# Performance work log

Measured on AMD Instinct MI355X. Metric: run time of the kernel, lower is better.

## Reference

```python
import jax, jax.numpy as jnp
import numpy as np

SR = 22050
FRAME_LENGTH = 64
ATTENUATE_GAIN = 0.02


def upsample_linear(x, scale):
    """torch nn.Upsample(mode='linear', align_corners=False) along last axis."""
    T = x.shape[-1]
    S = T * scale
    # source coordinate for each output sample (half-pixel convention), clamped
    coords = jnp.clip((jnp.arange(S, dtype=jnp.float32) + 0.5) / scale - 0.5, 0.0, T - 1)
    i0 = jnp.floor(coords).astype(jnp.int32)
    i1 = jnp.minimum(i0 + 1, T - 1)
    w = (coords - i0).astype(x.dtype)
    return x[..., i0] * (1.0 - w) + x[..., i1] * w


def setup_inputs() -> dict:
    key = jax.random.key(0)
    k1, k2, k3 = jax.random.split(key, 3)
    B, T, P, STR = 16, 1000, 64, 6
    # fundamental frequencies in [50, 450] Hz so high partials hit the Nyquist mask
    six_f0 = jax.random.uniform(k1, (B, T, STR), dtype=jnp.float32) * 400.0 + 50.0
    c = jax.random.uniform(k2, (STR, B, P, T), dtype=jnp.float32)
    a = jax.random.uniform(k3, (STR, B, T), dtype=jnp.float32)
    return {"six_f0": six_f0, "c": c, "a": a, "string_idx": 1}


def reference(six_f0, c, a, string_idx):
    sidx = string_idx - 1
    fundamentals = six_f0[..., sidx]        # (B, T)
    c_bank = c[sidx]                        # (B, P, T)
    loudness = a[sidx]                      # (B, T)
    P = c_bank.shape[1]

    partial_mult = jnp.arange(1, P + 1, dtype=jnp.float32)[:, None]   # (P, 1)
    f0_bank = fundamentals[:, None, :] * partial_mult                  # (B, P, T)
    mask = (f0_bank < SR / 2).astype(c_bank.dtype)
    c_masked = c_bank * mask

    f0_up = upsample_linear(f0_bank, FRAME_LENGTH)                     # (B, P, S)
    phase = jnp.cumsum(f0_up / SR, axis=2)
    a_up = upsample_linear(c_masked, FRAME_LENGTH)                     # (B, P, S)
    sinusoid_bank = jnp.sin(2.0 * np.pi * phase) * a_up * ATTENUATE_GAIN

    loudness_up = upsample_linear(loudness, FRAME_LENGTH)              # (B, S)
    return jnp.sum(sinusoid_bank, axis=1) * loudness_up                # (B, S)
```

## Files before the change

### kernel.cpp

```cpp
#include <hip/hip_runtime.h>
#include <math.h>

constexpr int B = 16, T = 1000, P = 64, STR = 6, SCALE = 64;
constexpr int S = T * SCALE;
constexpr int SEG_PITCH = 1024;
constexpr int SEGS_PER_BLK = 16;
constexpr int NF = 17;
constexpr int NBLK = 63;
#define NYQ 11025.0f
#define INV_SR (1.0f / 22050.0f)

__device__ __forceinline__ float fracf_(float x) {
#if __has_builtin(__builtin_amdgcn_fractf)
  return __builtin_amdgcn_fractf(x);
#else
  return x - floorf(x);
#endif
}
__device__ __forceinline__ float sin2pi(float r) {
#if __has_builtin(__builtin_amdgcn_sinf)
  return __builtin_amdgcn_sinf(r);
#else
  return __sinf(r * 6.28318530717958647692f);
#endif
}
__device__ __forceinline__ float cos2pi(float r) {
#if __has_builtin(__builtin_amdgcn_cosf)
  return __builtin_amdgcn_cosf(r);
#else
  return __cosf(r * 6.28318530717958647692f);
#endif
}

__global__ __launch_bounds__(256) void k_segbase(
    const float* __restrict__ six_f0, const int* __restrict__ sidx_p,
    float* __restrict__ segbase) {
  const int b = blockIdx.x;
  const int tid = threadIdx.x;
  const int sidx = sidx_p[0] - 1;

  __shared__ float Fs[T];
  for (int t = tid; t < T; t += 256)
    Fs[t] = six_f0[(size_t)(b * T + t) * STR + sidx];
  __syncthreads();

  double loc[4];
  double run = 0.0;
#pragma unroll
  for (int j = 0; j < 4; ++j) {
    int g = 4 * tid + j;
    double ssum = 0.0;
    if (g == 0)
      ssum = 32.0 * (double)Fs[0];
    else if (g <= T - 1)
      ssum = 32.0 * ((double)Fs[g - 1] + (double)Fs[g]);
    else if (g == T)
      ssum = 32.0 * (double)Fs[T - 1];
    loc[j] = run;
    run += ssum;
  }

  const int lane = tid & 63, wid = tid >> 6;
  double v = run;
  for (int off = 1; off < 64; off <<= 1) {
    double n = __shfl_up(v, off, 64);
    if (lane >= off) v += n;
  }
  __shared__ double wtot[4];
  if (lane == 63) wtot[wid] = v;
  __syncthreads();
  double excl = v - run;
  for (int w = 0; w < wid; ++w) excl += wtot[w];

#pragma unroll
  for (int j = 0; j < 4; ++j) {
    int g = 4 * tid + j;
    if (g <= T) {
      double ph = (excl + loc[j]) / 22050.0;
      ph -= floor(ph);
      segbase[b * SEG_PITCH + g] = (float)ph;
    }
  }
}

__global__ __launch_bounds__(256) void k_synth(
    const float* __restrict__ six_f0, const float* __restrict__ c,
    const float* __restrict__ a, const int* __restrict__ sidx_p,
    const float* __restrict__ segbase, float* __restrict__ out) {
  const int b = blockIdx.y;
  const int G0 = blockIdx.x * SEGS_PER_BLK;
  const int fbase = G0 - 1;
  const int tid = threadIdx.x;
  const int sidx = sidx_p[0] - 1;
  const float* cb = c + (size_t)sidx * B * P * T;
  const float* loud = a + (size_t)sidx * B * T + (size_t)b * T;

  __shared__ float Fsh[NF];
  __shared__ float Lsh[NF];
  __shared__ float ampsT[P][NF + 1];

  if (tid < NF) {
    int f = min(max(fbase + tid, 0), T - 1);
    Fsh[tid] = six_f0[(size_t)(b * T + f) * STR + sidx];
  } else if (tid < 2 * NF) {
    int i = tid - NF;
    int f = min(max(fbase + i, 0), T - 1);
    Lsh[i] = loud[f];
  }
  __syncthreads();

  for (int i = tid; i < P * NF; i += 256) {
    int p = i / NF, fl = i - p * NF;
    int f = min(max(fbase + fl, 0), T - 1);
    float F = Fsh[fl];
    float cv = cb[((size_t)b * P + p) * T + f];
    ampsT[p][fl] = ((float)(p + 1) * F < NYQ) ? cv : 0.0f;
  }
  __syncthreads();

  const int seg = G0 + (tid >> 4);
  const int q = tid & 15;
  const int lo_l = tid >> 4;
  const float Flo = Fsh[lo_l];
  const float Fhi = Fsh[lo_l + 1];
  const float Llo = Lsh[lo_l];
  const float dL = Lsh[lo_l + 1] - Llo;
  const float dF = Fhi - Flo;
  const float base = segbase[b * SEG_PITCH + min(seg, SEG_PITCH - 1)];
  const int kadj = (seg == 0) ? -32 : 0;
  const int kp = q * 4;

  float wj[4], twoC[4], scur[4], sprev[4], accj[4];
#pragma unroll
  for (int j = 0; j < 4; ++j) {
    int k = kp + j + kadj;
    float kf1 = (float)(k + 1);
    float local = (kf1 * Flo + dF * kf1 * kf1 * (1.0f / 128.0f)) * INV_SR;
    float phi = fracf_(base + local);
    wj[j] = ((float)k + 0.5f) * (1.0f / 64.0f);
    twoC[j] = 2.0f * cos2pi(phi);
    scur[j] = sin2pi(phi);
    sprev[j] = 0.0f;
    accj[j] = 0.0f;
  }

  const float Fmn = fminf(Flo, Fhi);
  const int pmax = min(P, (int)(NYQ / Fmn) + 1);

  const float* row = &ampsT[0][lo_l];
#pragma unroll 2
  for (int p = 0; p < pmax; ++p) {
    float a0 = row[p * (NF + 1)];
    float a1 = row[p * (NF + 1) + 1];
    float d = a1 - a0;
#pragma unroll
    for (int j = 0; j < 4; ++j) {
      float amp = fmaf(wj[j], d, a0);
      accj[j] = fmaf(amp, scur[j], accj[j]);
      float sn = fmaf(twoC[j], scur[j], -sprev[j]);
      sprev[j] = scur[j];
      scur[j] = sn;
    }
  }

  bool live = (seg < 1000) ? !(seg == 0 && q < 8) : (seg == 1000 && q < 8);
  if (live) {
    int s0 = seg * 64 - 32 + kp;
    float4 r;
    r.x = accj[0] * 0.02f * fmaf(wj[0], dL, Llo);
    r.y = accj[1] * 0.02f * fmaf(wj[1], dL, Llo);
    r.z = accj[2] * 0.02f * fmaf(wj[2], dL, Llo);
    r.w = accj[3] * 0.02f * fmaf(wj[3], dL, Llo);
    *(float4*)(out + (size_t)b * S + s0) = r;
  }
}

extern "C" void kernel_launch(void* const* d_in, const int* in_sizes, int n_in,
                              void* d_out, int out_size, void* d_ws,
                              size_t ws_size, hipStream_t stream) {
  const float* six_f0 = (const float*)d_in[0];
  const float* c = (const float*)d_in[1];
  const float* a = (const float*)d_in[2];
  const int* sidx = (const int*)d_in[3];
  float* out = (float*)d_out;
  float* segbase = (float*)d_ws;

  hipLaunchKernelGGL(k_segbase, dim3(B), dim3(256), 0, stream, six_f0, sidx,
                     segbase);
  hipLaunchKernelGGL(k_synth, dim3(NBLK, B), dim3(256), 0, stream, six_f0, c,
                     a, sidx, segbase, out);
}
```

Measured before the change: 87.30 us.

## Fuse phase prefix-sum into synthesis kernel, recomputing segment base per block

Drops the separate segment-base scan kernel. Each synthesis block now sums the strided f0 values before its first segment with a block-wide double reduction. Each thread then adds the per-segment increments up to its own segment to get its starting phase. This removes one kernel launch and the workspace round trip between the kernels. In exchange there is redundant prefix work: later blocks read up to about a thousand strided f0 values, plus a serial loop of up to 15 double additions per thread.

```diff
diff --git a/kernel.cpp b/kernel.cpp
--- a/kernel.cpp
+++ b/kernel.cpp
@@ -3,12 +3,12 @@
 
 constexpr int B = 16, T = 1000, P = 64, STR = 6, SCALE = 64;
 constexpr int S = T * SCALE;
-constexpr int SEG_PITCH = 1024;
 constexpr int SEGS_PER_BLK = 16;
 constexpr int NF = 17;
 constexpr int NBLK = 63;
 #define NYQ 11025.0f
 #define INV_SR (1.0f / 22050.0f)
+#define INV_SR_D (1.0 / 22050.0)
 
 __device__ __forceinline__ float fracf_(float x) {
 #if __has_builtin(__builtin_amdgcn_fractf)
@@ -32,81 +32,35 @@
 #endif
 }
 
-__global__ __launch_bounds__(256) void k_segbase(
-    const float* __restrict__ six_f0, const int* __restrict__ sidx_p,
-    float* __restrict__ segbase) {
-  const int b = blockIdx.x;
-  const int tid = threadIdx.x;
-  const int sidx = sidx_p[0] - 1;
-
-  __shared__ float Fs[T];
-  for (int t = tid; t < T; t += 256)
-    Fs[t] = six_f0[(size_t)(b * T + t) * STR + sidx];
-  __syncthreads();
-
-  double loc[4];
-  double run = 0.0;
-#pragma unroll
-  for (int j = 0; j < 4; ++j) {
-    int g = 4 * tid + j;
-    double ssum = 0.0;
-    if (g == 0)
-      ssum = 32.0 * (double)Fs[0];
-    else if (g <= T - 1)
-      ssum = 32.0 * ((double)Fs[g - 1] + (double)Fs[g]);
-    else if (g == T)
-      ssum = 32.0 * (double)Fs[T - 1];
-    loc[j] = run;
-    run += ssum;
-  }
-
-  const int lane = tid & 63, wid = tid >> 6;
-  double v = run;
-  for (int off = 1; off < 64; off <<= 1) {
-    double n = __shfl_up(v, off, 64);
-    if (lane >= off) v += n;
-  }
-  __shared__ double wtot[4];
-  if (lane == 63) wtot[wid] = v;
-  __syncthreads();
-  double excl = v - run;
-  for (int w = 0; w < wid; ++w) excl += wtot[w];
-
-#pragma unroll
-  for (int j = 0; j < 4; ++j) {
-    int g = 4 * tid + j;
-    if (g <= T) {
-      double ph = (excl + loc[j]) / 22050.0;
-      ph -= floor(ph);
-      segbase[b * SEG_PITCH + g] = (float)ph;
-    }
-  }
-}
-
-__global__ __launch_bounds__(256) void k_synth(
+__global__ __launch_bounds__(256) void k_fused(
     const float* __restrict__ six_f0, const float* __restrict__ c,
     const float* __restrict__ a, const int* __restrict__ sidx_p,
-    const float* __restrict__ segbase, float* __restrict__ out) {
+    float* __restrict__ out) {
   const int b = blockIdx.y;
   const int G0 = blockIdx.x * SEGS_PER_BLK;
   const int fbase = G0 - 1;
   const int tid = threadIdx.x;
   const int sidx = sidx_p[0] - 1;
+  const float* f0row = six_f0 + (size_t)b * T * STR + sidx;
   const float* cb = c + (size_t)sidx * B * P * T;
   const float* loud = a + (size_t)sidx * B * T + (size_t)b * T;
 
   __shared__ float Fsh[NF];
   __shared__ float Lsh[NF];
+  __shared__ double wtot[4];
   __shared__ float ampsT[P][NF + 1];
 
   if (tid < NF) {
     int f = min(max(fbase + tid, 0), T - 1);
-    Fsh[tid] = six_f0[(size_t)(b * T + f) * STR + sidx];
+    Fsh[tid] = f0row[(size_t)f * STR];
   } else if (tid < 2 * NF) {
     int i = tid - NF;
     int f = min(max(fbase + i, 0), T - 1);
     Lsh[i] = loud[f];
   }
+  double psum = 0.0;
+  for (int t = 1 + tid; t <= G0 - 2; t += 256)
+    psum += (double)f0row[(size_t)t * STR];
   __syncthreads();
 
   for (int i = tid; i < P * NF; i += 256) {
@@ -116,17 +70,46 @@
     float cv = cb[((size_t)b * P + p) * T + f];
     ampsT[p][fl] = ((float)(p + 1) * F < NYQ) ? cv : 0.0f;
   }
+  {
+    double v = psum;
+    for (int off = 32; off >= 1; off >>= 1) v += __shfl_down(v, off, 64);
+    if ((tid & 63) == 0) wtot[tid >> 6] = v;
+  }
   __syncthreads();
 
-  const int seg = G0 + (tid >> 4);
+  const double Ssum = wtot[0] + wtot[1] + wtot[2] + wtot[3];
+  const double F0d = (double)f0row[0];
+  double baseHz;
+  if (G0 == 0)
+    baseHz = 0.0;
+  else if (G0 == 1)
+    baseHz = 32.0 * F0d;
+  else
+    baseHz = 32.0 * F0d + 32.0 * (F0d + 2.0 * Ssum + (double)Fsh[0]);
+
+  const int m = tid >> 4;
+  const int seg = G0 + m;
+  for (int g = G0; g < seg; ++g) {
+    double ss;
+    if (g == 0)
+      ss = 32.0 * F0d;
+    else if (g >= T)
+      ss = 32.0 * (double)Fsh[g - 1 - fbase];
+    else
+      ss = 32.0 * ((double)Fsh[g - 1 - fbase] + (double)Fsh[g - fbase]);
+    baseHz += ss;
+  }
+  double phd = baseHz * INV_SR_D;
+  phd -= floor(phd);
+  const float base = (float)phd;
+
   const int q = tid & 15;
-  const int lo_l = tid >> 4;
+  const int lo_l = m;
   const float Flo = Fsh[lo_l];
   const float Fhi = Fsh[lo_l + 1];
   const float Llo = Lsh[lo_l];
   const float dL = Lsh[lo_l + 1] - Llo;
   const float dF = Fhi - Flo;
-  const float base = segbase[b * SEG_PITCH + min(seg, SEG_PITCH - 1)];
   const int kadj = (seg == 0) ? -32 : 0;
   const int kp = q * 4;
 
@@ -183,10 +166,7 @@
   const float* a = (const float*)d_in[2];
   const int* sidx = (const int*)d_in[3];
   float* out = (float*)d_out;
-  float* segbase = (float*)d_ws;
 
-  hipLaunchKernelGGL(k_segbase, dim3(B), dim3(256), 0, stream, six_f0, sidx,
-                     segbase);
-  hipLaunchKernelGGL(k_synth, dim3(NBLK, B), dim3(256), 0, stream, six_f0, c,
-                     a, sidx, segbase, out);
+  hipLaunchKernelGGL(k_fused, dim3(NBLK, B), dim3(256), 0, stream, six_f0, c,
+                     a, sidx, out);
 }
```

New measurement: 86.17 us. About the same (-1.3%).
